# Optimization experiments

Hardware: AMD Instinct MI355X
Metric: run time of the kernel (lower is better)

Reference implementation:

```python
import jax, jax.numpy as jnp
import numpy as np

T, B, DIN, DH, DOUT = 512, 256, 128, 512, 128


def setup_inputs() -> dict:
    key = jax.random.key(0)
    k1, k2, k3, k4 = jax.random.split(key, 4)
    xs = jax.random.normal(k1, (T, B, DIN), dtype=jnp.float32)
    W1x = 0.1 * jax.random.normal(k2, (DIN, DH), dtype=jnp.float32)
    # random orthogonal init for the recurrent weight, as in the original
    q, _ = jnp.linalg.qr(jax.random.normal(k3, (DH, DH), dtype=jnp.float32))
    W1h = q.astype(jnp.float32)
    b1 = jnp.zeros([], dtype=jnp.float32)
    W2 = 0.1 * jax.random.normal(k4, (DH, DOUT), dtype=jnp.float32)
    b2 = jnp.zeros([], dtype=jnp.float32)
    return {"xs": xs, "W1x": W1x, "W1h": W1h, "b1": b1, "W2": W2, "b2": b2}


def reference(xs, W1x, W1h, b1, W2, b2):
    # Precompute all input projections in one big GEMM: [T, B, DH]
    xproj = jnp.einsum('tbi,ih->tbh', xs, W1x)
    h0 = jnp.zeros((xs.shape[1], W1h.shape[0]), dtype=xs.dtype)

    def step(h, xp):
        h_new = jnp.tanh(xp + h @ W1h + b1)
        return h_new, None

    h_final, _ = jax.lax.scan(step, h0, xproj)
    return h_final @ W2 + b2
```

## Files before the change

kernel.cpp:

```cpp
#include <hip/hip_runtime.h>

#define T_STEPS 512
#define BATCH   256
#define DIN     128
#define DH      512
#define DOUT    128
#define RGRP    16

typedef __attribute__((ext_vector_type(8))) short  short8;
typedef __attribute__((ext_vector_type(4))) float  floatx4;
typedef __attribute__((ext_vector_type(4))) unsigned short ushort4v;

union Pack8 { short8 s; unsigned short h[8]; };

__device__ __forceinline__ float bf2f(unsigned short u) {
    union { unsigned int i; float f; } v; v.i = ((unsigned int)u) << 16; return v.f;
}
__device__ __forceinline__ unsigned short f2bf(float f) {
    union { float f; unsigned int i; } v; v.f = f;
    unsigned int b = v.i;
    b += 0x7FFFu + ((b >> 16) & 1u);
    return (unsigned short)(b >> 16);
}
__device__ __forceinline__ float fast_tanh(float v) {
    float ex = __expf(v + v);
    return 1.f - 2.f / (ex + 1.f);
}

__global__ void pack_b_kernel(const float* __restrict__ W,
                              unsigned short* __restrict__ Wp, int K, int N) {
    int idx = blockIdx.x * blockDim.x + threadIdx.x;
    if (idx >= K * N) return;
    int k = idx / N, n = idx % N;
    int nt = n >> 4, kc = k >> 5, quad = (k >> 3) & 3, j = k & 7;
    int lane = quad * 16 + (n & 15);
    int KC = K >> 5;
    Wp[((size_t)(nt * KC + kc) * 64 + lane) * 8 + j] = f2bf(W[idx]);
}

__global__ __launch_bounds__(256) void xproj_kernel(
        const float* __restrict__ xs,
        const unsigned short* __restrict__ W1xp,
        const float* __restrict__ b1p,
        unsigned short* __restrict__ xpe) {
    const int tid  = threadIdx.x;
    const int lane = tid & 63;
    const int w    = tid >> 6;
    const int m    = lane & 15;
    const int q    = lane >> 4;
    const long row0 = (long)blockIdx.x * 16;
    const float b1 = b1p[0];

    short8 a[4];
#pragma unroll
    for (int kc = 0; kc < 4; ++kc) {
        const float* src = xs + (row0 + m) * DIN + kc * 32 + q * 8;
        Pack8 av;
#pragma unroll
        for (int j = 0; j < 8; ++j) av.h[j] = f2bf(src[j]);
        a[kc] = av.s;
    }

#pragma unroll
    for (int i = 0; i < 8; ++i) {
        const int nt = w * 8 + i;
        floatx4 acc = {0.f, 0.f, 0.f, 0.f};
#pragma unroll
        for (int kc = 0; kc < 4; ++kc) {
            short8 b = *(const short8*)(W1xp + ((size_t)(nt * 4 + kc) * 64 + lane) * 8);
            acc = __builtin_amdgcn_mfma_f32_16x16x32_bf16(a[kc], b, acc, 0, 0, 0);
        }
        ushort4v sv;
#pragma unroll
        for (int r = 0; r < 4; ++r) sv[r] = f2bf(acc[r] + b1);
        *(ushort4v*)&xpe[((size_t)blockIdx.x * 512 +
                          (size_t)(nt >> 2) * 64 + lane) * 16 + (nt & 3) * 4] = sv;
    }
}

template <int LKC>
__global__ __launch_bounds__(512) __attribute__((amdgpu_waves_per_eu(2, 2)))
void rnn_agpr(const unsigned short* __restrict__ xpe,
              const unsigned short* __restrict__ W1hp,
              const float* __restrict__ W2,
              const float* __restrict__ b2p,
              float* __restrict__ out) {
    extern __shared__ unsigned short smem[];
    unsigned short* Hb = smem;
    unsigned short* Wl = smem + 16384;

    const int tid  = threadIdx.x;
    const int lane = tid & 63;
    const int w    = tid >> 6;
    const int m    = lane & 15;
    const int q    = lane >> 4;
    const int rg   = blockIdx.x;

    constexpr int RKC  = 8;
    constexpr int SKC0 = RKC + LKC;
    constexpr int NS   = 16 - RKC - LKC;
    constexpr int NG   = NS / 2;

    short8 wa[RKC][4];
#pragma unroll
    for (int kc = 0; kc < RKC; ++kc)
#pragma unroll
        for (int i = 0; i < 4; ++i) {
            wa[kc][i] = *(const short8*)(W1hp +
                ((size_t)((4 * w + i) * 16 + kc) * 64 + lane) * 8);
            asm("" : "+a"(wa[kc][i]));
        }

    if (LKC > 0) {
        for (int c = tid; c < LKC * 2048; c += 512) {
            int j = c >> 11;
            int r2 = c & 2047;
            int nt = r2 >> 6, ln = r2 & 63;
            *(short8*)&Wl[(size_t)c * 8] =
                *(const short8*)(W1hp + ((size_t)(nt * 16 + RKC + j) * 64 + ln) * 8);
        }
    }

    const int slot = lane ^ ((lane >> 4) << 2) ^ (((lane >> 3) & 1) << 1);
    int roff = slot * 8;

    int widx[4];
#pragma unroll
    for (int i = 0; i < 4; ++i) {
        int kcp = 2 * w + (i >> 1);
        int qp  = (2 * i + (m >> 3)) & 3;
        int lp  = 4 * q + 16 * qp;
        int sl  = lp ^ ((lp >> 4) << 2) ^ (((lp >> 3) & 1) << 1);
        widx[i] = kcp * 512 + sl * 8 + (m & 7);
    }

    {
        const unsigned short* xb =
            xpe + ((size_t)rg * 512 + (size_t)w * 64 + lane) * 16;
        Pack8 x0, x1;
        x0.s = ((const short8*)xb)[0];
        x1.s = ((const short8*)xb)[1];
#pragma unroll
        for (int i = 0; i < 4; ++i) {
            Pack8 xh = (i < 2) ? x0 : x1;
#pragma unroll
            for (int r = 0; r < 4; ++r) {
                float v = bf2f(xh.h[(i & 1) * 4 + r]);
                Hb[widx[i] ^ (r << 3)] = f2bf(fast_tanh(v));
            }
            widx[i] ^= 8192;
        }
    }
    __syncthreads();

#pragma unroll 1
    for (int t = 1; t < T_STEPS; ++t) {
        asm volatile("" ::: "memory");

        const unsigned short* hrd = Hb + roff;

        short8 sb[2][4];
#pragma unroll
        for (int c = 0; c < 2; ++c)
#pragma unroll
            for (int i = 0; i < 4; ++i)
                sb[c][i] = *(const short8*)(W1hp +
                    ((size_t)((4 * w + i) * 16 + SKC0 + c) * 64 + lane) * 8);

        Pack8 x0, x1;
        {
            const unsigned short* xb = xpe +
                (((size_t)t * 16 + rg) * 512 + (size_t)w * 64 + lane) * 16;
            x0.s = ((const short8*)xb)[0];
            x1.s = ((const short8*)xb)[1];
        }

        floatx4 acc[4];
#pragma unroll
        for (int i = 0; i < 4; ++i) acc[i] = (floatx4){0.f, 0.f, 0.f, 0.f};

#pragma unroll
        for (int kc = 0; kc < RKC; ++kc) {
            short8 a = *(const short8*)&hrd[kc * 512];
#pragma unroll
            for (int i = 0; i < 4; ++i)
                asm("v_mfma_f32_16x16x32_bf16 %0, %1, %2, %0"
                    : "+v"(acc[i]) : "v"(a), "a"(wa[kc][i]));
        }

#pragma unroll
        for (int g = 0; g < NG; ++g) {
#pragma unroll
            for (int c = 0; c < 2; ++c) {
                short8 a = *(const short8*)&hrd[(SKC0 + 2 * g + c) * 512];
#pragma unroll
                for (int i = 0; i < 4; ++i)
                    acc[i] = __builtin_amdgcn_mfma_f32_16x16x32_bf16(a, sb[c][i], acc[i], 0, 0, 0);
            }
            if (g + 1 < NG) {
#pragma unroll
                for (int c = 0; c < 2; ++c)
#pragma unroll
                    for (int i = 0; i < 4; ++i)
                        sb[c][i] = *(const short8*)(W1hp +
                            ((size_t)((4 * w + i) * 16 + SKC0 + 2 * (g + 1) + c) * 64 + lane) * 8);
            }
            if (g == 0 && LKC > 0) {
#pragma unroll
                for (int j = 0; j < LKC; ++j) {
                    short8 a = *(const short8*)&hrd[(RKC + j) * 512];
#pragma unroll
                    for (int i = 0; i < 4; ++i) {
                        short8 b = *(const short8*)&Wl[((size_t)(j * 32 + 4 * w + i) * 64 + lane) * 8];
                        acc[i] = __builtin_amdgcn_mfma_f32_16x16x32_bf16(a, b, acc[i], 0, 0, 0);
                    }
                }
            }
        }

#pragma unroll
        for (int i = 0; i < 4; ++i) {
            Pack8 xh = (i < 2) ? x0 : x1;
#pragma unroll
            for (int r = 0; r < 4; ++r) {
                float v = acc[i][r] + bf2f(xh.h[(i & 1) * 4 + r]);
                Hb[widx[i] ^ (r << 3)] = f2bf(fast_tanh(v));
            }
            widx[i] ^= 8192;
        }
        roff ^= 8192;
        __syncthreads();
    }

    const float b2 = b2p[0];
    floatx4 acc = {0.f, 0.f, 0.f, 0.f};
#pragma unroll
    for (int kc = 0; kc < 16; ++kc) {
        short8 av = *(const short8*)&Hb[roff + kc * 512];
        Pack8 bv;
#pragma unroll
        for (int j = 0; j < 8; ++j)
            bv.h[j] = f2bf(W2[(size_t)(kc * 32 + q * 8 + j) * DOUT + w * 16 + m]);
        acc = __builtin_amdgcn_mfma_f32_16x16x32_bf16(av, bv.s, acc, 0, 0, 0);
    }
#pragma unroll
    for (int r = 0; r < 4; ++r)
        out[(size_t)(rg * 16 + q * 4 + r) * DOUT + w * 16 + m] = acc[r] + b2;
}

extern "C" void kernel_launch(void* const* d_in, const int* in_sizes, int n_in,
                              void* d_out, int out_size, void* d_ws, size_t ws_size,
                              hipStream_t stream) {
    const float* xs  = (const float*)d_in[0];
    const float* W1x = (const float*)d_in[1];
    const float* W1h = (const float*)d_in[2];
    const float* b1  = (const float*)d_in[3];
    const float* W2  = (const float*)d_in[4];
    const float* b2  = (const float*)d_in[5];
    float* out = (float*)d_out;

    unsigned short* xpe  = (unsigned short*)d_ws;
    unsigned short* w1hp = xpe + (size_t)T_STEPS * BATCH * DH;
    unsigned short* w1xp = w1hp + (size_t)DH * DH;

    pack_b_kernel<<<(DH * DH + 255) / 256, 256, 0, stream>>>(W1h, w1hp, DH, DH);
    pack_b_kernel<<<(DIN * DH + 255) / 256, 256, 0, stream>>>(W1x, w1xp, DIN, DH);
    xproj_kernel<<<(T_STEPS * BATCH) / 16, 256, 0, stream>>>(xs, w1xp, b1, xpe);

    constexpr size_t SMEM_BIG   = 32768 + 4 * 32768;
    constexpr size_t SMEM_SMALL = 32768;
    hipError_t e = hipFuncSetAttribute(
        reinterpret_cast<const void*>(&rnn_agpr<4>),
        hipFuncAttributeMaxDynamicSharedMemorySize, (int)SMEM_BIG);
    if (e == hipSuccess) {
        rnn_agpr<4><<<RGRP, 512, SMEM_BIG, stream>>>(xpe, w1hp, W2, b2, out);
    } else {
        rnn_agpr<0><<<RGRP, 512, SMEM_SMALL, stream>>>(xpe, w1hp, W2, b2, out);
    }
}
```

Baseline: 1.825 ms.

## Restructure recurrent step tail to overlap per-tile tanh epilogue with remaining MFMAs

Rewrites the streamed-weight part of the recurrent step. Each timestep now uses a rotating k-chunk order (offset by t), preloads the streamed W1h chunks for output tiles 0-1 up front, and splits the last four k-chunks per output tile. This lets each tile's tanh and shared-memory store start while later tiles' MFMAs are still pending. The aim is to hide epilogue latency and spread global and LDS accesses across banks and channels. It also removes the compiler memory barrier at the top of the loop, and the extra register pressure from preloading 8 short8 values may affect scheduling.

```diff
diff --git a/kernel.cpp b/kernel.cpp
--- a/kernel.cpp
+++ b/kernel.cpp
@@ -80,11 +80,11 @@
 
 template <int LKC>
 __global__ __launch_bounds__(512) __attribute__((amdgpu_waves_per_eu(2, 2)))
-void rnn_agpr(const unsigned short* __restrict__ xpe,
-              const unsigned short* __restrict__ W1hp,
-              const float* __restrict__ W2,
-              const float* __restrict__ b2p,
-              float* __restrict__ out) {
+void rnn_v5(const unsigned short* __restrict__ xpe,
+            const unsigned short* __restrict__ W1hp,
+            const float* __restrict__ W2,
+            const float* __restrict__ b2p,
+            float* __restrict__ out) {
     extern __shared__ unsigned short smem[];
     unsigned short* Hb = smem;
     unsigned short* Wl = smem + 16384;
@@ -96,10 +96,7 @@
     const int q    = lane >> 4;
     const int rg   = blockIdx.x;
 
-    constexpr int RKC  = 8;
-    constexpr int SKC0 = RKC + LKC;
-    constexpr int NS   = 16 - RKC - LKC;
-    constexpr int NG   = NS / 2;
+    constexpr int RKC = 8;
 
     short8 wa[RKC][4];
 #pragma unroll
@@ -155,17 +152,17 @@
 
 #pragma unroll 1
     for (int t = 1; t < T_STEPS; ++t) {
-        asm volatile("" ::: "memory");
-
         const unsigned short* hrd = Hb + roff;
 
-        short8 sb[2][4];
-#pragma unroll
-        for (int c = 0; c < 2; ++c)
-#pragma unroll
-            for (int i = 0; i < 4; ++i)
-                sb[c][i] = *(const short8*)(W1hp +
-                    ((size_t)((4 * w + i) * 16 + SKC0 + c) * 64 + lane) * 8);
+        short8 sb0[4], sb1[4];
+#pragma unroll
+        for (int c = 0; c < 4; ++c) {
+            int kc = 12 + ((c + t) & 3);
+            sb0[c] = *(const short8*)(W1hp +
+                ((size_t)((4 * w + 0) * 16 + kc) * 64 + lane) * 8);
+            sb1[c] = *(const short8*)(W1hp +
+                ((size_t)((4 * w + 1) * 16 + kc) * 64 + lane) * 8);
+        }
 
         Pack8 x0, x1;
         {
@@ -188,46 +185,78 @@
                     : "+v"(acc[i]) : "v"(a), "a"(wa[kc][i]));
         }
 
-#pragma unroll
-        for (int g = 0; g < NG; ++g) {
-#pragma unroll
-            for (int c = 0; c < 2; ++c) {
-                short8 a = *(const short8*)&hrd[(SKC0 + 2 * g + c) * 512];
-#pragma unroll
-                for (int i = 0; i < 4; ++i)
-                    acc[i] = __builtin_amdgcn_mfma_f32_16x16x32_bf16(a, sb[c][i], acc[i], 0, 0, 0);
-            }
-            if (g + 1 < NG) {
-#pragma unroll
-                for (int c = 0; c < 2; ++c)
-#pragma unroll
-                    for (int i = 0; i < 4; ++i)
-                        sb[c][i] = *(const short8*)(W1hp +
-                            ((size_t)((4 * w + i) * 16 + SKC0 + 2 * (g + 1) + c) * 64 + lane) * 8);
-            }
-            if (g == 0 && LKC > 0) {
-#pragma unroll
-                for (int j = 0; j < LKC; ++j) {
-                    short8 a = *(const short8*)&hrd[(RKC + j) * 512];
-#pragma unroll
-                    for (int i = 0; i < 4; ++i) {
-                        short8 b = *(const short8*)&Wl[((size_t)(j * 32 + 4 * w + i) * 64 + lane) * 8];
-                        acc[i] = __builtin_amdgcn_mfma_f32_16x16x32_bf16(a, b, acc[i], 0, 0, 0);
-                    }
+        if (LKC > 0) {
+#pragma unroll
+            for (int j = 0; j < 4; ++j) {
+                int jr = (j + t) & 3;
+                short8 a = *(const short8*)&hrd[(RKC + jr) * 512];
+#pragma unroll
+                for (int i = 0; i < 4; ++i) {
+                    short8 b = *(const short8*)&Wl[((size_t)(jr * 32 + 4 * w + i) * 64 + lane) * 8];
+                    acc[i] = __builtin_amdgcn_mfma_f32_16x16x32_bf16(a, b, acc[i], 0, 0, 0);
                 }
             }
-        }
-
-#pragma unroll
-        for (int i = 0; i < 4; ++i) {
-            Pack8 xh = (i < 2) ? x0 : x1;
-#pragma unroll
-            for (int r = 0; r < 4; ++r) {
-                float v = acc[i][r] + bf2f(xh.h[(i & 1) * 4 + r]);
-                Hb[widx[i] ^ (r << 3)] = f2bf(fast_tanh(v));
+        } else {
+#pragma unroll
+            for (int c = 0; c < 4; ++c) {
+                int kc = 8 + ((c + t) & 3);
+                short8 a = *(const short8*)&hrd[kc * 512];
+#pragma unroll
+                for (int i = 0; i < 4; ++i) {
+                    short8 b = *(const short8*)(W1hp +
+                        ((size_t)((4 * w + i) * 16 + kc) * 64 + lane) * 8);
+                    acc[i] = __builtin_amdgcn_mfma_f32_16x16x32_bf16(a, b, acc[i], 0, 0, 0);
+                }
             }
-            widx[i] ^= 8192;
-        }
+        }
+
+        short8 at[4];
+#pragma unroll
+        for (int c = 0; c < 4; ++c)
+            at[c] = *(const short8*)&hrd[(12 + ((c + t) & 3)) * 512];
+
+        short8 sb2[4], sb3[4];
+#pragma unroll
+        for (int c = 0; c < 4; ++c) {
+            int kc = 12 + ((c + t) & 3);
+            sb2[c] = *(const short8*)(W1hp +
+                ((size_t)((4 * w + 2) * 16 + kc) * 64 + lane) * 8);
+            sb3[c] = *(const short8*)(W1hp +
+                ((size_t)((4 * w + 3) * 16 + kc) * 64 + lane) * 8);
+        }
+
+#pragma unroll
+        for (int c = 0; c < 4; ++c)
+            acc[0] = __builtin_amdgcn_mfma_f32_16x16x32_bf16(at[c], sb0[c], acc[0], 0, 0, 0);
+#pragma unroll
+        for (int r = 0; r < 4; ++r)
+            Hb[widx[0] ^ (r << 3)] = f2bf(fast_tanh(acc[0][r] + bf2f(x0.h[r])));
+        widx[0] ^= 8192;
+
+#pragma unroll
+        for (int c = 0; c < 4; ++c)
+            acc[1] = __builtin_amdgcn_mfma_f32_16x16x32_bf16(at[c], sb1[c], acc[1], 0, 0, 0);
+#pragma unroll
+        for (int r = 0; r < 4; ++r)
+            Hb[widx[1] ^ (r << 3)] = f2bf(fast_tanh(acc[1][r] + bf2f(x0.h[4 + r])));
+        widx[1] ^= 8192;
+
+#pragma unroll
+        for (int c = 0; c < 4; ++c)
+            acc[2] = __builtin_amdgcn_mfma_f32_16x16x32_bf16(at[c], sb2[c], acc[2], 0, 0, 0);
+#pragma unroll
+        for (int r = 0; r < 4; ++r)
+            Hb[widx[2] ^ (r << 3)] = f2bf(fast_tanh(acc[2][r] + bf2f(x1.h[r])));
+        widx[2] ^= 8192;
+
+#pragma unroll
+        for (int c = 0; c < 4; ++c)
+            acc[3] = __builtin_amdgcn_mfma_f32_16x16x32_bf16(at[c], sb3[c], acc[3], 0, 0, 0);
+#pragma unroll
+        for (int r = 0; r < 4; ++r)
+            Hb[widx[3] ^ (r << 3)] = f2bf(fast_tanh(acc[3][r] + bf2f(x1.h[4 + r])));
+        widx[3] ^= 8192;
+
         roff ^= 8192;
         __syncthreads();
     }
@@ -270,11 +299,11 @@
     constexpr size_t SMEM_BIG   = 32768 + 4 * 32768;
     constexpr size_t SMEM_SMALL = 32768;
     hipError_t e = hipFuncSetAttribute(
-        reinterpret_cast<const void*>(&rnn_agpr<4>),
+        reinterpret_cast<const void*>(&rnn_v5<4>),
         hipFuncAttributeMaxDynamicSharedMemorySize, (int)SMEM_BIG);
     if (e == hipSuccess) {
-        rnn_agpr<4><<<RGRP, 512, SMEM_BIG, stream>>>(xpe, w1hp, W2, b2, out);
+        rnn_v5<4><<<RGRP, 512, SMEM_BIG, stream>>>(xpe, w1hp, W2, b2, out);
     } else {
-        rnn_agpr<0><<<RGRP, 512, SMEM_SMALL, stream>>>(xpe, w1hp, W2, b2, out);
-    }
-}
+        rnn_v5<0><<<RGRP, 512, SMEM_SMALL, stream>>>(xpe, w1hp, W2, b2, out);
+    }
+}
```

After: 1.788 ms. 1.02x faster.

## Halve recurrent kernel to 256 threads with 8 N-tiles per wave

Applied to the files above, without the earlier changes.

The recurrent kernel now runs 4 waves per block instead of 8, and each wave computes 8 output tiles, so every LDS read of the hidden-state A fragment feeds twice as many MFMAs. Register-resident W1h chunks drop from 8 to 6 K-chunks but cover 8 tiles each, and LDS-resident weight chunks drop from 4 to 2. The remaining chunks are streamed from global memory with a per-timestep rotation, so different blocks touch different cache lines at any moment. This cuts LDS traffic and barrier participants per step, at the cost of more global weight streaming, higher register pressure and fewer waves to hide latency.

```diff
diff --git a/kernel.cpp b/kernel.cpp
--- a/kernel.cpp
+++ b/kernel.cpp
@@ -79,12 +79,12 @@
 }
 
 template <int LKC>
-__global__ __launch_bounds__(512) __attribute__((amdgpu_waves_per_eu(2, 2)))
-void rnn_agpr(const unsigned short* __restrict__ xpe,
-              const unsigned short* __restrict__ W1hp,
-              const float* __restrict__ W2,
-              const float* __restrict__ b2p,
-              float* __restrict__ out) {
+__global__ __launch_bounds__(256, 1)
+void rnn_v9(const unsigned short* __restrict__ xpe,
+            const unsigned short* __restrict__ W1hp,
+            const float* __restrict__ W2,
+            const float* __restrict__ b2p,
+            float* __restrict__ out) {
     extern __shared__ unsigned short smem[];
     unsigned short* Hb = smem;
     unsigned short* Wl = smem + 16384;
@@ -96,24 +96,23 @@
     const int q    = lane >> 4;
     const int rg   = blockIdx.x;
 
-    constexpr int RKC  = 8;
+    constexpr int RKC  = 6;
     constexpr int SKC0 = RKC + LKC;
     constexpr int NS   = 16 - RKC - LKC;
-    constexpr int NG   = NS / 2;
-
-    short8 wa[RKC][4];
+
+    short8 wa[RKC][8];
 #pragma unroll
     for (int kc = 0; kc < RKC; ++kc)
 #pragma unroll
-        for (int i = 0; i < 4; ++i) {
+        for (int i = 0; i < 8; ++i) {
             wa[kc][i] = *(const short8*)(W1hp +
-                ((size_t)((4 * w + i) * 16 + kc) * 64 + lane) * 8);
+                ((size_t)((8 * w + i) * 16 + kc) * 64 + lane) * 8);
             asm("" : "+a"(wa[kc][i]));
         }
 
     if (LKC > 0) {
-        for (int c = tid; c < LKC * 2048; c += 512) {
-            int j = c >> 11;
+        for (int c = tid; c < LKC * 2048; c += 256) {
+            int j  = c >> 11;
             int r2 = c & 2047;
             int nt = r2 >> 6, ln = r2 & 63;
             *(short8*)&Wl[(size_t)c * 8] =
@@ -124,10 +123,10 @@
     const int slot = lane ^ ((lane >> 4) << 2) ^ (((lane >> 3) & 1) << 1);
     int roff = slot * 8;
 
-    int widx[4];
-#pragma unroll
-    for (int i = 0; i < 4; ++i) {
-        int kcp = 2 * w + (i >> 1);
+    int widx[8];
+#pragma unroll
+    for (int i = 0; i < 8; ++i) {
+        int kcp = 4 * w + (i >> 1);
         int qp  = (2 * i + (m >> 3)) & 3;
         int lp  = 4 * q + 16 * qp;
         int sl  = lp ^ ((lp >> 4) << 2) ^ (((lp >> 3) & 1) << 1);
@@ -135,17 +134,21 @@
     }
 
     {
-        const unsigned short* xb =
-            xpe + ((size_t)rg * 512 + (size_t)w * 64 + lane) * 16;
-        Pack8 x0, x1;
-        x0.s = ((const short8*)xb)[0];
-        x1.s = ((const short8*)xb)[1];
-#pragma unroll
-        for (int i = 0; i < 4; ++i) {
-            Pack8 xh = (i < 2) ? x0 : x1;
+        short8 xq[2][2];
+#pragma unroll
+        for (int g = 0; g < 2; ++g) {
+            const unsigned short* xb =
+                xpe + ((size_t)rg * 512 + (size_t)(2 * w + g) * 64 + lane) * 16;
+            xq[g][0] = ((const short8*)xb)[0];
+            xq[g][1] = ((const short8*)xb)[1];
+        }
+#pragma unroll
+        for (int i = 0; i < 8; ++i) {
+            int g = i >> 2, ci = i & 3;
+            Pack8 ph; ph.s = xq[g][ci >> 1];
 #pragma unroll
             for (int r = 0; r < 4; ++r) {
-                float v = bf2f(xh.h[(i & 1) * 4 + r]);
+                float v = bf2f(ph.h[(ci & 1) * 4 + r]);
                 Hb[widx[i] ^ (r << 3)] = f2bf(fast_tanh(v));
             }
             widx[i] ^= 8192;
@@ -155,75 +158,81 @@
 
 #pragma unroll 1
     for (int t = 1; t < T_STEPS; ++t) {
-        asm volatile("" ::: "memory");
+#pragma unroll
+        for (int kc = 0; kc < RKC; ++kc)
+#pragma unroll
+            for (int i = 0; i < 8; ++i)
+                asm("" : "+a"(wa[kc][i]));
 
         const unsigned short* hrd = Hb + roff;
-
-        short8 sb[2][4];
-#pragma unroll
-        for (int c = 0; c < 2; ++c)
-#pragma unroll
-            for (int i = 0; i < 4; ++i)
+        const int rot = t % NS;
+
+        short8 sb[2][8];
+#pragma unroll
+        for (int c = 0; c < 2; ++c) {
+            int x = c + rot; if (x >= NS) x -= NS;
+            const int kc = SKC0 + x;
+#pragma unroll
+            for (int i = 0; i < 8; ++i)
                 sb[c][i] = *(const short8*)(W1hp +
-                    ((size_t)((4 * w + i) * 16 + SKC0 + c) * 64 + lane) * 8);
-
-        Pack8 x0, x1;
-        {
+                    ((size_t)((8 * w + i) * 16 + kc) * 64 + lane) * 8);
+        }
+
+        short8 xq[2][2];
+#pragma unroll
+        for (int g = 0; g < 2; ++g) {
             const unsigned short* xb = xpe +
-                (((size_t)t * 16 + rg) * 512 + (size_t)w * 64 + lane) * 16;
-            x0.s = ((const short8*)xb)[0];
-            x1.s = ((const short8*)xb)[1];
-        }
-
-        floatx4 acc[4];
-#pragma unroll
-        for (int i = 0; i < 4; ++i) acc[i] = (floatx4){0.f, 0.f, 0.f, 0.f};
+                (((size_t)t * 16 + rg) * 512 + (size_t)(2 * w + g) * 64 + lane) * 16;
+            xq[g][0] = ((const short8*)xb)[0];
+            xq[g][1] = ((const short8*)xb)[1];
+        }
+
+        floatx4 acc[8];
+#pragma unroll
+        for (int i = 0; i < 8; ++i) acc[i] = (floatx4){0.f, 0.f, 0.f, 0.f};
 
 #pragma unroll
         for (int kc = 0; kc < RKC; ++kc) {
             short8 a = *(const short8*)&hrd[kc * 512];
 #pragma unroll
-            for (int i = 0; i < 4; ++i)
-                asm("v_mfma_f32_16x16x32_bf16 %0, %1, %2, %0"
-                    : "+v"(acc[i]) : "v"(a), "a"(wa[kc][i]));
-        }
-
-#pragma unroll
-        for (int g = 0; g < NG; ++g) {
-#pragma unroll
-            for (int c = 0; c < 2; ++c) {
-                short8 a = *(const short8*)&hrd[(SKC0 + 2 * g + c) * 512];
-#pragma unroll
-                for (int i = 0; i < 4; ++i)
-                    acc[i] = __builtin_amdgcn_mfma_f32_16x16x32_bf16(a, sb[c][i], acc[i], 0, 0, 0);
-            }
-            if (g + 1 < NG) {
-#pragma unroll
-                for (int c = 0; c < 2; ++c)
-#pragma unroll
-                    for (int i = 0; i < 4; ++i)
-                        sb[c][i] = *(const short8*)(W1hp +
-                            ((size_t)((4 * w + i) * 16 + SKC0 + 2 * (g + 1) + c) * 64 + lane) * 8);
-            }
-            if (g == 0 && LKC > 0) {
-#pragma unroll
-                for (int j = 0; j < LKC; ++j) {
-                    short8 a = *(const short8*)&hrd[(RKC + j) * 512];
-#pragma unroll
-                    for (int i = 0; i < 4; ++i) {
-                        short8 b = *(const short8*)&Wl[((size_t)(j * 32 + 4 * w + i) * 64 + lane) * 8];
-                        acc[i] = __builtin_amdgcn_mfma_f32_16x16x32_bf16(a, b, acc[i], 0, 0, 0);
-                    }
-                }
-            }
-        }
-
-#pragma unroll
-        for (int i = 0; i < 4; ++i) {
-            Pack8 xh = (i < 2) ? x0 : x1;
+            for (int i = 0; i < 8; ++i)
+                acc[i] = __builtin_amdgcn_mfma_f32_16x16x32_bf16(a, wa[kc][i], acc[i], 0, 0, 0);
+        }
+
+#pragma unroll
+        for (int j = 0; j < LKC; ++j) {
+            short8 a = *(const short8*)&hrd[(RKC + j) * 512];
+#pragma unroll
+            for (int i = 0; i < 8; ++i) {
+                short8 b = *(const short8*)&Wl[((size_t)(j * 32 + 8 * w + i) * 64 + lane) * 8];
+                acc[i] = __builtin_amdgcn_mfma_f32_16x16x32_bf16(a, b, acc[i], 0, 0, 0);
+            }
+        }
+
+#pragma unroll
+        for (int sc = 0; sc < NS; ++sc) {
+            int xa = sc + rot; if (xa >= NS) xa -= NS;
+            short8 a = *(const short8*)&hrd[(SKC0 + xa) * 512];
+#pragma unroll
+            for (int i = 0; i < 8; ++i)
+                acc[i] = __builtin_amdgcn_mfma_f32_16x16x32_bf16(a, sb[sc & 1][i], acc[i], 0, 0, 0);
+            if (sc + 2 < NS) {
+                int x = sc + 2 + rot; if (x >= NS) x -= NS;
+                const int kc = SKC0 + x;
+#pragma unroll
+                for (int i = 0; i < 8; ++i)
+                    sb[sc & 1][i] = *(const short8*)(W1hp +
+                        ((size_t)((8 * w + i) * 16 + kc) * 64 + lane) * 8);
+            }
+        }
+
+#pragma unroll
+        for (int i = 0; i < 8; ++i) {
+            const int g = i >> 2, ci = i & 3;
+            Pack8 ph; ph.s = xq[g][ci >> 1];
 #pragma unroll
             for (int r = 0; r < 4; ++r) {
-                float v = acc[i][r] + bf2f(xh.h[(i & 1) * 4 + r]);
+                float v = acc[i][r] + bf2f(ph.h[(ci & 1) * 4 + r]);
                 Hb[widx[i] ^ (r << 3)] = f2bf(fast_tanh(v));
             }
             widx[i] ^= 8192;
@@ -233,19 +242,23 @@
     }
 
     const float b2 = b2p[0];
-    floatx4 acc = {0.f, 0.f, 0.f, 0.f};
-#pragma unroll
-    for (int kc = 0; kc < 16; ++kc) {
-        short8 av = *(const short8*)&Hb[roff + kc * 512];
-        Pack8 bv;
-#pragma unroll
-        for (int j = 0; j < 8; ++j)
-            bv.h[j] = f2bf(W2[(size_t)(kc * 32 + q * 8 + j) * DOUT + w * 16 + m]);
-        acc = __builtin_amdgcn_mfma_f32_16x16x32_bf16(av, bv.s, acc, 0, 0, 0);
-    }
-#pragma unroll
-    for (int r = 0; r < 4; ++r)
-        out[(size_t)(rg * 16 + q * 4 + r) * DOUT + w * 16 + m] = acc[r] + b2;
+#pragma unroll
+    for (int w2t = 0; w2t < 2; ++w2t) {
+        const int w2 = 2 * w + w2t;
+        floatx4 acc2 = {0.f, 0.f, 0.f, 0.f};
+#pragma unroll
+        for (int kc = 0; kc < 16; ++kc) {
+            short8 av = *(const short8*)&Hb[roff + kc * 512];
+            Pack8 bv;
+#pragma unroll
+            for (int j = 0; j < 8; ++j)
+                bv.h[j] = f2bf(W2[(size_t)(kc * 32 + q * 8 + j) * DOUT + w2 * 16 + m]);
+            acc2 = __builtin_amdgcn_mfma_f32_16x16x32_bf16(av, bv.s, acc2, 0, 0, 0);
+        }
+#pragma unroll
+        for (int r = 0; r < 4; ++r)
+            out[(size_t)(rg * 16 + q * 4 + r) * DOUT + w2 * 16 + m] = acc2[r] + b2;
+    }
 }
 
 extern "C" void kernel_launch(void* const* d_in, const int* in_sizes, int n_in,
@@ -267,14 +280,14 @@
     pack_b_kernel<<<(DIN * DH + 255) / 256, 256, 0, stream>>>(W1x, w1xp, DIN, DH);
     xproj_kernel<<<(T_STEPS * BATCH) / 16, 256, 0, stream>>>(xs, w1xp, b1, xpe);
 
-    constexpr size_t SMEM_BIG   = 32768 + 4 * 32768;
+    constexpr size_t SMEM_BIG   = 32768 + 2 * 32768;
     constexpr size_t SMEM_SMALL = 32768;
     hipError_t e = hipFuncSetAttribute(
-        reinterpret_cast<const void*>(&rnn_agpr<4>),
+        reinterpret_cast<const void*>(&rnn_v9<2>),
         hipFuncAttributeMaxDynamicSharedMemorySize, (int)SMEM_BIG);
     if (e == hipSuccess) {
-        rnn_agpr<4><<<RGRP, 512, SMEM_BIG, stream>>>(xpe, w1hp, W2, b2, out);
+        rnn_v9<2><<<RGRP, 256, SMEM_BIG, stream>>>(xpe, w1hp, W2, b2, out);
     } else {
-        rnn_agpr<0><<<RGRP, 512, SMEM_SMALL, stream>>>(xpe, w1hp, W2, b2, out);
-    }
-}
+        rnn_v9<0><<<RGRP, 256, SMEM_SMALL, stream>>>(xpe, w1hp, W2, b2, out);
+    }
+}
```

After: 2.180 ms. +19.4%, slower.
